# Kernel tuning notes

Measured on AMD Instinct MI355X. Metric: run time of the kernel, lower is better.

The kernel has to match this reference:

```python
import jax, jax.numpy as jnp
import numpy as np

DIM = 128; D_STATE = 16; D_CONV = 4; EXPAND = 2
D_INNER = DIM * EXPAND            # 256
DT_RANK = (DIM + 15) // 16        # 8
B, H, W = 2, 56, 56


def _ln(x, w, b):
    m = jnp.mean(x, -1, keepdims=True)
    v = jnp.var(x, -1, keepdims=True)
    return (x - m) * jax.lax.rsqrt(v + 1e-5) * w + b


def _mamba(x, in_w, conv_w, conv_b, xproj_w, dt_w, dt_b, A_log, Dp, out_w):
    # x: (B, L, DIM)
    Bb, L, _ = x.shape
    xz = x @ in_w.T                                   # (B,L,2*D_INNER)
    xi, z = jnp.split(xz, 2, axis=-1)
    # causal depthwise conv1d (pad left d_conv-1, truncate to L)
    xc = jnp.transpose(xi, (0, 2, 1))                 # (B,D_INNER,L)
    xc = jax.lax.conv_general_dilated(
        xc, conv_w, (1,), [(D_CONV - 1, 0)],
        dimension_numbers=('NCH', 'OIH', 'NCH'),
        feature_group_count=D_INNER) + conv_b[None, :, None]
    xs = jax.nn.silu(jnp.transpose(xc, (0, 2, 1)))    # (B,L,D_INNER)
    dbl = xs @ xproj_w.T                              # (B,L,DT_RANK+2*D_STATE)
    dt = jax.nn.softplus(dbl[..., :DT_RANK] @ dt_w.T + dt_b)   # (B,L,D_INNER)
    Bc = dbl[..., DT_RANK:DT_RANK + D_STATE]          # (B,L,D_STATE)
    Cc = dbl[..., DT_RANK + D_STATE:]                 # (B,L,D_STATE)
    A = -jnp.exp(A_log)                               # (D_INNER,D_STATE)
    dA = jnp.exp(dt[..., None] * A)                   # (B,L,D_INNER,D_STATE)
    dBu = (dt * xs)[..., None] * Bc[:, :, None, :]    # (B,L,D_INNER,D_STATE)

    def step(h, inp):
        a, bu, c = inp
        h = a * h + bu                                # (B,D_INNER,D_STATE)
        return h, jnp.einsum('bdn,bn->bd', h, c)

    h0 = jnp.zeros((Bb, D_INNER, D_STATE), x.dtype)
    _, ys = jax.lax.scan(step, h0, (jnp.moveaxis(dA, 1, 0),
                                    jnp.moveaxis(dBu, 1, 0),
                                    jnp.moveaxis(Cc, 1, 0)))
    y = jnp.moveaxis(ys, 0, 1) + xs * Dp              # (B,L,D_INNER)
    y = y * jax.nn.silu(z)
    return y @ out_w.T                                # (B,L,DIM)


def _forward(x, norm_h_w, norm_h_b, norm_v_w, norm_v_b,
             dw_w, dw_b, pw_w, pw_b,
             h_in_w, h_conv_w, h_conv_b, h_xproj_w, h_dt_w, h_dt_b, h_A_log, h_D, h_out_w,
             v_in_w, v_conv_w, v_conv_b, v_xproj_w, v_dt_w, v_dt_b, v_A_log, v_D, v_out_w,
             ca_fc1_w, ca_fc2_w):
    Bb, C, Hh, Ww = x.shape
    # local branch: depthwise 3x3 + GELU + 1x1
    lf = jax.lax.conv_general_dilated(
        x, dw_w, (1, 1), [(1, 1), (1, 1)],
        dimension_numbers=('NCHW', 'OIHW', 'NCHW'),
        feature_group_count=C) + dw_b[None, :, None, None]
    lf = jax.nn.gelu(lf, approximate=False)
    lf = jnp.einsum('bchw,oc->bohw', lf, pw_w[:, :, 0, 0]) + pw_b[None, :, None, None]
    # horizontal scan: row-major tokens
    xh = _ln(x.reshape(Bb, C, Hh * Ww).transpose(0, 2, 1), norm_h_w, norm_h_b)
    oh = _mamba(xh, h_in_w, h_conv_w, h_conv_b, h_xproj_w, h_dt_w, h_dt_b,
                h_A_log, h_D, h_out_w)
    oh = oh.transpose(0, 2, 1).reshape(Bb, C, Hh, Ww)
    # vertical scan: column-major tokens
    xv = _ln(jnp.transpose(x, (0, 1, 3, 2)).reshape(Bb, C, Ww * Hh).transpose(0, 2, 1),
             norm_v_w, norm_v_b)
    ov = _mamba(xv, v_in_w, v_conv_w, v_conv_b, v_xproj_w, v_dt_w, v_dt_b,
                v_A_log, v_D, v_out_w)
    ov = jnp.transpose(ov.transpose(0, 2, 1).reshape(Bb, C, Ww, Hh), (0, 1, 3, 2))
    fused = oh + ov + lf
    # channel attention
    y = jnp.mean(fused, axis=(2, 3))                  # (B,C)
    y = jax.nn.sigmoid(jax.nn.relu(y @ ca_fc1_w.T) @ ca_fc2_w.T)
    return fused * y[:, :, None, None] + x


def setup_inputs() -> dict:
    key = jax.random.key(0)
    ks = iter(jax.random.split(key, 64))
    def nrm(shape, scale):
        return jax.random.normal(next(ks), shape, jnp.float32) * scale
    d = {}
    d['x'] = nrm((B, DIM, H, W), 1.0)
    d['norm_h_w'] = jnp.ones((DIM,), jnp.float32); d['norm_h_b'] = jnp.zeros((DIM,), jnp.float32)
    d['norm_v_w'] = jnp.ones((DIM,), jnp.float32); d['norm_v_b'] = jnp.zeros((DIM,), jnp.float32)
    d['dw_w'] = nrm((DIM, 1, 3, 3), 1.0 / 3.0)
    d['dw_b'] = jnp.zeros((DIM,), jnp.float32)
    d['pw_w'] = nrm((DIM, DIM, 1, 1), DIM ** -0.5)
    d['pw_b'] = jnp.zeros((DIM,), jnp.float32)
    for p in ('h', 'v'):
        d[p + '_in_w'] = nrm((2 * D_INNER, DIM), DIM ** -0.5)
        d[p + '_conv_w'] = nrm((D_INNER, 1, D_CONV), D_CONV ** -0.5)
        d[p + '_conv_b'] = jnp.zeros((D_INNER,), jnp.float32)
        d[p + '_xproj_w'] = nrm((DT_RANK + 2 * D_STATE, D_INNER), D_INNER ** -0.5)
        d[p + '_dt_w'] = nrm((D_INNER, DT_RANK), DT_RANK ** -0.5)
        d[p + '_dt_b'] = jnp.full((D_INNER,), -2.0, jnp.float32)  # small positive dt
        d[p + '_A_log'] = jnp.log(jnp.tile(jnp.arange(1, D_STATE + 1, dtype=jnp.float32), (D_INNER, 1)))
        d[p + '_D'] = jnp.ones((D_INNER,), jnp.float32)
        d[p + '_out_w'] = nrm((DIM, D_INNER), D_INNER ** -0.5)
    d['ca_fc1_w'] = nrm((DIM // 4, DIM), DIM ** -0.5)
    d['ca_fc2_w'] = nrm((DIM, DIM // 4), (DIM // 4) ** -0.5)
    return d


def reference(x, norm_h_w, norm_h_b, norm_v_w, norm_v_b,
              dw_w, dw_b, pw_w, pw_b,
              h_in_w, h_conv_w, h_conv_b, h_xproj_w, h_dt_w, h_dt_b, h_A_log, h_D, h_out_w,
              v_in_w, v_conv_w, v_conv_b, v_xproj_w, v_dt_w, v_dt_b, v_A_log, v_D, v_out_w,
              ca_fc1_w, ca_fc2_w):
    return _forward(x, norm_h_w, norm_h_b, norm_v_w, norm_v_b,
                    dw_w, dw_b, pw_w, pw_b,
                    h_in_w, h_conv_w, h_conv_b, h_xproj_w, h_dt_w, h_dt_b, h_A_log, h_D, h_out_w,
                    v_in_w, v_conv_w, v_conv_b, v_xproj_w, v_dt_w, v_dt_b, v_A_log, v_D, v_out_w,
                    ca_fc1_w, ca_fc2_w)
```

## Files before the change

kernel.cpp:

```cpp
#include <hip/hip_runtime.h>
#include <hip/hip_bf16.h>

typedef __hip_bfloat16 bf16;
__device__ __forceinline__ float b2f(bf16 v){ return __bfloat162float(v); }
__device__ __forceinline__ bf16 f2b(float v){ return __float2bfloat16(v); }

typedef __attribute__((ext_vector_type(8))) short frag_ab;
typedef __attribute__((ext_vector_type(4))) float frag_cd;
typedef __attribute__((ext_vector_type(4))) short short4v;

__device__ __forceinline__ frag_ab ld_frag_2xb64(const bf16* p){
  union { frag_ab f; short4v h[2]; } u;
  u.h[0] = *reinterpret_cast<const short4v*>(p);
  u.h[1] = *reinterpret_cast<const short4v*>(p+4);
  return u.f;
}

#define LLEN 3136
#define BATCH 2
#define NCHUNK 49
#define LC 64

__global__ void k_dwconv_gelu(const float* __restrict__ x, const float* __restrict__ dww,
                              const float* __restrict__ dwb, bf16* __restrict__ tmp,
                              float* __restrict__ YMEAN){
  int bc = blockIdx.x;
  int c = bc & 127;
  if (bc == 0 && blockIdx.y == 0 && threadIdx.x < 256) YMEAN[threadIdx.x] = 0.f;
  const float* xp = x + (size_t)bc*LLEN;
  float w[9];
  #pragma unroll
  for (int i=0;i<9;i++) w[i] = dww[c*9+i];
  float bias = dwb[c];
  int pstart = blockIdx.y * 784;
  int pend = pstart + 784;
  for (int p = pstart + threadIdx.x; p < pend; p += 256){
    int i = p/56, j = p%56;
    float acc = bias;
    #pragma unroll
    for (int a=0;a<3;a++){
      int ii = i + a - 1;
      if (ii < 0 || ii >= 56) continue;
      #pragma unroll
      for (int bb=0;bb<3;bb++){
        int jj = j + bb - 1;
        if (jj < 0 || jj >= 56) continue;
        acc += w[a*3+bb] * xp[ii*56+jj];
      }
    }
    float g = 0.5f*acc*(1.0f + erff(acc*0.70710678118654752f));
    tmp[(size_t)bc*LLEN + p] = f2b(g);
  }
}

__global__ void k_ln(const float* __restrict__ x, const float* nhw_, const float* nhb_,
                     const float* nvw_, const float* nvb_, bf16* __restrict__ xln){
  __shared__ float sx[128][57];
  __shared__ float smean[56], srstd[56];
  __shared__ float wh[128], bh[128], wv_[128], bv_[128];
  int h = blockIdx.x; int b = blockIdx.y;
  int tid = threadIdx.x;
  if (tid < 128){ wh[tid]=nhw_[tid]; bh[tid]=nhb_[tid];
                  wv_[tid]=nvw_[tid]; bv_[tid]=nvb_[tid]; }
  for (int idx = tid; idx < 128*56; idx += 256){
    int c = idx / 56, w = idx % 56;
    sx[c][w] = x[((size_t)(b*128+c))*LLEN + h*56 + w];
  }
  __syncthreads();
  if (tid < 56){
    float s=0.f, s2=0.f;
    for (int c=0;c<128;c++){ float v = sx[c][tid]; s+=v; s2+=v*v; }
    float m = s*(1.f/128.f);
    float var = s2*(1.f/128.f) - m*m;
    smean[tid]=m; srstd[tid]=rsqrtf(var+1e-5f);
  }
  __syncthreads();
  bf16* outh = xln;
  bf16* outv = xln + (size_t)BATCH*LLEN*128;
  for (int idx = tid; idx < 56*128; idx += 256){
    int w = idx >> 7, c = idx & 127;
    float v = (sx[c][w]-smean[w])*srstd[w];
    outh[((size_t)b*LLEN + h*56 + w)*128 + c] = f2b(v*wh[c]+bh[c]);
    outv[((size_t)b*LLEN + w*56 + h)*128 + c] = f2b(v*wv_[c]+bv_[c]);
  }
}

__global__ void k_inproj(const bf16* __restrict__ xln, const float* __restrict__ hw,
                         const float* __restrict__ vw, bf16* __restrict__ XI, bf16* __restrict__ Z){
  int dir = blockIdx.z;
  const bf16* A = xln + (size_t)dir*BATCH*LLEN*128;
  const float* W = dir ? vw : hw;
  int m0 = blockIdx.x*64, n0 = blockIdx.y*64;
  __shared__ __align__(16) bf16 sA[64][136];
  __shared__ __align__(16) bf16 sW[64][136];
  int tid = threadIdx.x;
  #pragma unroll
  for (int r=0;r<4;r++){
    int idx = tid + r*256;
    int row = idx >> 4, c8 = (idx & 15)*8;
    *reinterpret_cast<float4*>(&sA[row][c8]) =
        *reinterpret_cast<const float4*>(&A[(size_t)(m0+row)*128 + c8]);
  }
  #pragma unroll
  for (int r=0;r<8;r++){
    int idx = tid + r*256;
    int row = idx >> 5, c4 = (idx & 31)*4;
    float4 w4 = *reinterpret_cast<const float4*>(&W[(size_t)(n0+row)*128 + c4]);
    bf16 t4[4] = {f2b(w4.x), f2b(w4.y), f2b(w4.z), f2b(w4.w)};
    *reinterpret_cast<double*>(&sW[row][c4]) = *reinterpret_cast<double*>(t4);
  }
  __syncthreads();
  int wv2 = tid >> 6, lane = tid & 63;
  int qd = lane >> 4, mr = lane & 15;
  frag_cd acc[4] = {};
  #pragma unroll
  for (int k0=0;k0<128;k0+=32){
    frag_ab af = *reinterpret_cast<frag_ab*>(&sA[wv2*16+mr][k0+qd*8]);
    #pragma unroll
    for (int t=0;t<4;t++){
      frag_ab bfr = *reinterpret_cast<frag_ab*>(&sW[t*16+mr][k0+qd*8]);
      acc[t] = __builtin_amdgcn_mfma_f32_16x16x32_bf16(af, bfr, acc[t], 0, 0, 0);
    }
  }
  bf16* dst = (n0 < 256) ? XI : Z;
  int nb = n0 & 255;
  size_t dslab = (size_t)dir*BATCH*LLEN*256;
  #pragma unroll
  for (int t=0;t<4;t++)
    #pragma unroll
    for (int r=0;r<4;r++){
      int row = m0 + wv2*16 + qd*4 + r;
      int col = nb + t*16 + mr;
      dst[dslab + (size_t)row*256 + col] = f2b(acc[t][r]);
    }
}

__global__ void k_conv(const bf16* __restrict__ XI, const float* hw, const float* hb,
                       const float* vw, const float* vb, bf16* __restrict__ XS2){
  int dir = blockIdx.z;
  int b = blockIdx.y;
  int bd = dir*BATCH + b;
  int l0 = blockIdx.x * 32;
  const bf16* XId = XI + (size_t)bd*LLEN*256;
  const float* cw = dir ? vw : hw;
  const float* cb = dir ? vb : hb;
  __shared__ float sxi[35][256];
  int tid = threadIdx.x;
  for (int r = 0; r < 35; r++){
    int l = l0 - 3 + r;
    sxi[r][tid] = (l >= 0) ? b2f(XId[(size_t)l*256 + tid]) : 0.f;
  }
  __syncthreads();
  float w0=cw[tid*4], w1=cw[tid*4+1], w2=cw[tid*4+2], w3=cw[tid*4+3];
  float bias = cb[tid];
  size_t x2base = ((size_t)bd*16 + (tid>>4))*LLEN;
  int c16 = tid & 15;
  for (int ll=0; ll<32; ll++){
    float acc = bias + w0*sxi[ll][tid] + w1*sxi[ll+1][tid] + w2*sxi[ll+2][tid] + w3*sxi[ll+3][tid];
    float s = acc / (1.f + __expf(-acc));
    XS2[(x2base + l0 + ll)*16 + c16] = f2b(s);
  }
}

__global__ void k_dbl(const bf16* __restrict__ XS2, const float* __restrict__ hx,
                      const float* __restrict__ vx,
                      const float* hdw, const float* vdw, const float* hdb, const float* vdb,
                      const float* hA, const float* vA,
                      bf16* __restrict__ DT2, float* __restrict__ Bf, float* __restrict__ Cf,
                      float* __restrict__ Pbuf, float* __restrict__ Hbuf){
  int m0 = blockIdx.x*64;
  int bd = m0 / LLEN;
  int l0m = m0 % LLEN;
  int ck = l0m / LC;
  int dirq = bd >> 1;
  const float* W = dirq ? vx : hx;
  __shared__ __align__(16) bf16 sA[64][264];
  __shared__ __align__(16) bf16 sW[48][264];
  __shared__ float sdbl[64][49];
  int tid = threadIdx.x;
  #pragma unroll
  for (int r=0;r<8;r++){
    int idx = tid + r*256;
    int row = idx >> 5, c8 = (idx & 31)*8;
    size_t src = (((size_t)bd*16 + (c8>>4))*LLEN + l0m + row)*16 + (c8&15);
    *reinterpret_cast<float4*>(&sA[row][c8]) =
        *reinterpret_cast<const float4*>(&XS2[src]);
  }
  #pragma unroll
  for (int r=0;r<12;r++){
    int idx = tid + r*256;
    int row = idx >> 6, c4 = (idx & 63)*4;
    bf16 t4[4] = {f2b(0.f), f2b(0.f), f2b(0.f), f2b(0.f)};
    if (row < 40){
      float4 w4 = *reinterpret_cast<const float4*>(&W[(size_t)row*256 + c4]);
      t4[0]=f2b(w4.x); t4[1]=f2b(w4.y); t4[2]=f2b(w4.z); t4[3]=f2b(w4.w);
    }
    *reinterpret_cast<double*>(&sW[row][c4]) = *reinterpret_cast<double*>(t4);
  }
  __syncthreads();
  int wv2 = tid >> 6, lane = tid & 63;
  int qd = lane >> 4, mr = lane & 15;
  frag_cd acc[3] = {};
  #pragma unroll
  for (int k0=0;k0<256;k0+=32){
    frag_ab af = *reinterpret_cast<frag_ab*>(&sA[wv2*16+mr][k0+qd*8]);
    #pragma unroll
    for (int t=0;t<3;t++){
      frag_ab bfr = *reinterpret_cast<frag_ab*>(&sW[t*16+mr][k0+qd*8]);
      acc[t] = __builtin_amdgcn_mfma_f32_16x16x32_bf16(af, bfr, acc[t], 0, 0, 0);
    }
  }
  #pragma unroll
  for (int t=0;t<3;t++)
    #pragma unroll
    for (int r=0;r<4;r++){
      int col = t*16 + mr;
      if (col < 40) sdbl[wv2*16 + qd*4 + r][col] = acc[t][r];
    }
  __syncthreads();
  const float* dtw = dirq ? vdw : hdw;
  const float* dtb = dirq ? vdb : hdb;
  const float* Alog = dirq ? vA : hA;
  float w8[8];
  #pragma unroll
  for (int r=0;r<8;r++) w8[r] = dtw[tid*8+r];
  float biasv = dtb[tid];
  float Aq[16];
  #pragma unroll
  for (int n=0;n<16;n++) Aq[n] = -__expf(Alog[tid*16+n]);
  float hst[16] = {};
  float Pst[16];
  #pragma unroll
  for (int n=0;n<16;n++) Pst[n] = 1.f;
  size_t d2base = ((size_t)bd*16 + (tid>>4))*LLEN + l0m;
  int c16 = tid & 15;
  for (int row=0; row<64; row++){
    float a = biasv;
    #pragma unroll
    for (int r=0;r<8;r++) a += sdbl[row][r]*w8[r];
    float sv = (a > 20.f) ? a : __logf(1.f + __expf(a));
    bf16 svb16 = f2b(sv);
    DT2[(d2base + row)*16 + c16] = svb16;
    float svb = b2f(svb16);
    float u = b2f(sA[row][tid]);
    float au = svb*u;
    #pragma unroll
    for (int n=0;n<16;n++){
      float dA = __expf(svb * Aq[n]);
      hst[n] = dA*hst[n] + au*sdbl[row][8+n];
      Pst[n] *= dA;
    }
  }
  size_t pbase = (((size_t)bd*16 + (tid>>4))*NCHUNK + ck)*256 + (size_t)(tid&15)*16;
  #pragma unroll
  for (int n=0;n<16;n++){ Pbuf[pbase+n] = Pst[n]; Hbuf[pbase+n] = hst[n]; }
  #pragma unroll
  for (int r=0;r<8;r++){
    int idx = tid + r*256;
    int row = idx >> 5, o = idx & 31;
    float v = sdbl[row][8+o];
    size_t rr = (size_t)(m0+row)*16;
    if (o < 16) Bf[rr + o] = v;
    else        Cf[rr + (o-16)] = v;
  }
}

__global__ void k_scan2(const float* __restrict__ Pbuf, float* __restrict__ Hbuf){
  int q = blockIdx.x;
  int tid = threadIdx.x;
  float carry = 0.f;
  for (int k=0;k<NCHUNK;k++){
    size_t idx = ((size_t)q*NCHUNK + k)*256 + tid;
    float Pv = Pbuf[idx];
    float He = Hbuf[idx];
    Hbuf[idx] = carry;
    carry = Pv*carry + He;
  }
}

__global__ void k_scan3(const bf16* __restrict__ DT2, const bf16* __restrict__ XS2,
                        const float* __restrict__ Bc, const float* __restrict__ Cc,
                        const float* hA, const float* vA,
                        const float* __restrict__ Hbuf, bf16* __restrict__ ys){
  int bd = blockIdx.z;
  int g  = blockIdx.y;
  int ck = blockIdx.x;
  int l0 = ck*LC;
  const float* Bd = Bc + (size_t)bd*LLEN*16;
  const float* Cd = Cc + (size_t)bd*LLEN*16;
  bf16* yd = ys + (size_t)bd*LLEN*256;
  const float* Alog = (bd >> 1) ? vA : hA;
  int tid = threadIdx.x;
  int dl = tid >> 4, n = tid & 15;
  float A = -__expf(Alog[(g*16+dl)*16+n]);
  __shared__ float sdt[LC][16], sxs[LC][16], sB[LC][16], sC[LC][16];
  __shared__ __align__(16) float sp2[16][276];
  size_t base2 = (((size_t)bd*16 + g)*LLEN + l0)*16;
  #pragma unroll
  for (int r=0;r<4;r++){
    int idx = tid + r*256;
    sdt[idx>>4][idx&15] = b2f(DT2[base2 + idx]);
    sxs[idx>>4][idx&15] = b2f(XS2[base2 + idx]);
    (&sB[0][0])[idx] = Bd[(size_t)l0*16 + idx];
    (&sC[0][0])[idx] = Cd[(size_t)l0*16 + idx];
  }
  size_t sidx = (((size_t)bd*16 + g)*NCHUNK + ck)*256 + tid;
  float h = Hbuf[sidx];
  __syncthreads();
  int i_local = tid >> 4;
  int c16 = tid & 15;
  for (int i0=0; i0<LC; i0+=16){
    #pragma unroll
    for (int ii=0;ii<16;ii++){
      int i = i0 + ii;
      float a = sdt[i][dl];
      float u = sxs[i][dl];
      float dA = __expf(a * A);
      h = dA*h + (a*u)*sB[i][n];
      sp2[ii][tid] = h * sC[i][n];
    }
    __syncthreads();
    const float* row = &sp2[i_local][c16*16];
    float s = 0.f;
    #pragma unroll
    for (int k=0;k<4;k++){
      float4 v = *reinterpret_cast<const float4*>(row + k*4);
      s += v.x + v.y + v.z + v.w;
    }
    yd[(size_t)(l0+i0+i_local)*256 + g*16 + c16] = f2b(s);
    __syncthreads();
  }
}

__global__ void k_outgemm(const bf16* __restrict__ ys, const bf16* __restrict__ XS2,
                          const bf16* __restrict__ Z, const float* __restrict__ hD,
                          const float* __restrict__ vD, const float* __restrict__ how,
                          const float* __restrict__ vow, bf16* __restrict__ OD){
  int dir = blockIdx.z;
  size_t slab = (size_t)dir*BATCH*LLEN*256;
  const float* W = dir ? vow : how;
  const float* Dw = dir ? vD : hD;
  bf16* od = OD + (size_t)dir*BATCH*LLEN*128;
  int m0 = blockIdx.x*64, n0 = blockIdx.y*64;
  int bd = dir*2 + m0/LLEN;
  int lbase = m0 % LLEN;
  __shared__ __align__(16) bf16 sA[64][136];
  __shared__ __align__(16) bf16 sW[64][136];
  int tid = threadIdx.x;
  int wv2 = tid >> 6, lane = tid & 63;
  int qd = lane >> 4, mr = lane & 15;
  frag_cd acc[4] = {};
  for (int kc=0; kc<256; kc+=128){
    __syncthreads();
    #pragma unroll
    for (int r=0;r<4;r++){
      int idx = tid + r*256;
      int row = idx >> 4, c8 = (idx & 15)*8;
      int k = kc + c8;
      size_t e = slab + (size_t)(m0+row)*256 + k;
      size_t e2 = (((size_t)bd*16 + (k>>4))*LLEN + lbase + row)*16 + (k&15);
      bf16 yb[8], xb[8], zb[8], ob[8];
      *reinterpret_cast<float4*>(yb) = *reinterpret_cast<const float4*>(&ys[e]);
      *reinterpret_cast<float4*>(xb) = *reinterpret_cast<const float4*>(&XS2[e2]);
      *reinterpret_cast<float4*>(zb) = *reinterpret_cast<const float4*>(&Z[e]);
      #pragma unroll
      for (int j=0;j<8;j++){
        float Dv = Dw[k + j];
        float yv = b2f(yb[j]) + b2f(xb[j])*Dv;
        float zv = b2f(zb[j]);
        ob[j] = f2b(yv * (zv/(1.f+__expf(-zv))));
      }
      *reinterpret_cast<float4*>(&sA[row][c8]) = *reinterpret_cast<float4*>(ob);
    }
    #pragma unroll
    for (int r=0;r<8;r++){
      int idx = tid + r*256;
      int row = idx >> 5, c4 = (idx & 31)*4;
      float4 w4 = *reinterpret_cast<const float4*>(&W[(size_t)(n0+row)*256 + kc + c4]);
      bf16 t4[4] = {f2b(w4.x), f2b(w4.y), f2b(w4.z), f2b(w4.w)};
      *reinterpret_cast<double*>(&sW[row][c4]) = *reinterpret_cast<double*>(t4);
    }
    __syncthreads();
    #pragma unroll
    for (int k0=0;k0<128;k0+=32){
      frag_ab af = *reinterpret_cast<frag_ab*>(&sA[wv2*16+mr][k0+qd*8]);
      #pragma unroll
      for (int t=0;t<4;t++){
        frag_ab bfr = *reinterpret_cast<frag_ab*>(&sW[t*16+mr][k0+qd*8]);
        acc[t] = __builtin_amdgcn_mfma_f32_16x16x32_bf16(af, bfr, acc[t], 0, 0, 0);
      }
    }
  }
  #pragma unroll
  for (int t=0;t<4;t++)
    #pragma unroll
    for (int r=0;r<4;r++){
      int row = m0 + wv2*16 + qd*4 + r;
      int col = n0 + t*16 + mr;
      od[(size_t)row*128 + col] = f2b(acc[t][r]);
    }
}

__global__ void k_pwcomb(const bf16* __restrict__ tmp, const float* __restrict__ pww,
                         const float* __restrict__ pwb, const bf16* __restrict__ OD,
                         float* __restrict__ fused, float* __restrict__ YMEAN){
  int p0 = blockIdx.x * 64;
  int m0 = blockIdx.y * 64;
  int b  = blockIdx.z;
  const bf16* T = tmp + (size_t)b*128*LLEN;
  const bf16* od0 = OD + (size_t)b*LLEN*128;
  const bf16* od1 = OD + (size_t)(BATCH + b)*LLEN*128;
  __shared__ __align__(16) bf16 sA[64][136];
  __shared__ __align__(16) bf16 sBt[64][132];
  __shared__ float sOD[64][65];
  int tid = threadIdx.x;
  #pragma unroll
  for (int r=0;r<8;r++){
    int idx = tid + r*256;
    int row = idx >> 5, c4 = (idx & 31)*4;
    float4 w4 = *reinterpret_cast<const float4*>(&pww[(size_t)(m0+row)*128 + c4]);
    bf16 t4[4] = {f2b(w4.x), f2b(w4.y), f2b(w4.z), f2b(w4.w)};
    *reinterpret_cast<double*>(&sA[row][c4]) = *reinterpret_cast<double*>(t4);
  }
  #pragma unroll
  for (int r=0;r<8;r++){
    int idx = tid + r*256;
    int c = idx >> 4, p4 = (idx & 15)*4;
    union { double d; bf16 v[4]; } u;
    u.d = *reinterpret_cast<const double*>(&T[(size_t)c*LLEN + p0 + p4]);
    #pragma unroll
    for (int j=0;j<4;j++) sBt[p4+j][c] = u.v[j];
  }
  #pragma unroll
  for (int r=0;r<8;r++){
    int idx = tid + r*256;
    int prow = idx >> 5, mp = (idx & 31)*2;
    int p = p0 + prow;
    int pi = p/56, pj = p%56;
    int pt = pj*56 + pi;
    bf16 a0[2], a1[2];
    *reinterpret_cast<float*>(a0) = *reinterpret_cast<const float*>(&od0[(size_t)p*128 + m0 + mp]);
    *reinterpret_cast<float*>(a1) = *reinterpret_cast<const float*>(&od1[(size_t)pt*128 + m0 + mp]);
    sOD[prow][mp]   = b2f(a0[0]) + b2f(a1[0]);
    sOD[prow][mp+1] = b2f(a0[1]) + b2f(a1[1]);
  }
  __syncthreads();
  int wv2 = tid >> 6, lane = tid & 63;
  int qd = lane >> 4, mr = lane & 15;
  frag_cd acc[4] = {};
  #pragma unroll
  for (int k0=0;k0<128;k0+=32){
    frag_ab af = *reinterpret_cast<frag_ab*>(&sA[wv2*16+mr][k0+qd*8]);
    #pragma unroll
    for (int t=0;t<4;t++){
      frag_ab bfr = ld_frag_2xb64(&sBt[t*16+mr][k0+qd*8]);
      acc[t] = __builtin_amdgcn_mfma_f32_16x16x32_bf16(af, bfr, acc[t], 0, 0, 0);
    }
  }
  #pragma unroll
  for (int r=0;r<4;r++){
    int m = m0 + wv2*16 + qd*4 + r;
    float bias = pwb[m];
    float s = 0.f;
    #pragma unroll
    for (int t=0;t<4;t++){
      int p = p0 + t*16 + mr;
      float val = acc[t][r] + bias + sOD[t*16+mr][m - m0];
      fused[((size_t)b*128 + m)*LLEN + p] = val;
      s += val;
    }
    s += __shfl_xor(s, 1, 16);
    s += __shfl_xor(s, 2, 16);
    s += __shfl_xor(s, 4, 16);
    s += __shfl_xor(s, 8, 16);
    if (mr == 0) atomicAdd(&YMEAN[b*128 + m], s);
  }
}

__global__ void k_final_gate(const float* __restrict__ fused, const float* __restrict__ YMEAN,
                             const float* __restrict__ fc1, const float* __restrict__ fc2,
                             const float* __restrict__ x, float* __restrict__ out){
  int bc = blockIdx.y;
  int b = bc >> 7, c = bc & 127;
  __shared__ float ym[128], s1[32];
  __shared__ float gsh;
  int tid = threadIdx.x;
  if (tid < 128) ym[tid] = YMEAN[b*128 + tid] * (1.f/(float)LLEN);
  __syncthreads();
  if (tid < 32){
    float a = 0.f;
    for (int cc=0;cc<128;cc++) a += ym[cc]*fc1[tid*128+cc];
    s1[tid] = fmaxf(a, 0.f);
  }
  __syncthreads();
  if (tid == 0){
    float a = 0.f;
    #pragma unroll
    for (int j=0;j<32;j++) a += s1[j]*fc2[c*32+j];
    gsh = 1.f/(1.f+__expf(-a));
  }
  __syncthreads();
  float g = gsh;
  int p = blockIdx.x*256 + tid;
  if (p < LLEN){
    size_t i = (size_t)bc*LLEN + p;
    out[i] = fused[i]*g + x[i];
  }
}

extern "C" void kernel_launch(void* const* d_in, const int* in_sizes, int n_in,
                              void* d_out, int out_size, void* d_ws, size_t ws_size,
                              hipStream_t stream) {
  const float* x      = (const float*)d_in[0];
  const float* nhw    = (const float*)d_in[1];
  const float* nhb    = (const float*)d_in[2];
  const float* nvw    = (const float*)d_in[3];
  const float* nvb    = (const float*)d_in[4];
  const float* dww    = (const float*)d_in[5];
  const float* dwb    = (const float*)d_in[6];
  const float* pww    = (const float*)d_in[7];
  const float* pwb    = (const float*)d_in[8];
  const float* h_inw  = (const float*)d_in[9];
  const float* h_cw   = (const float*)d_in[10];
  const float* h_cb   = (const float*)d_in[11];
  const float* h_xw   = (const float*)d_in[12];
  const float* h_dtw  = (const float*)d_in[13];
  const float* h_dtb  = (const float*)d_in[14];
  const float* h_Al   = (const float*)d_in[15];
  const float* h_D    = (const float*)d_in[16];
  const float* h_ow   = (const float*)d_in[17];
  const float* v_inw  = (const float*)d_in[18];
  const float* v_cw   = (const float*)d_in[19];
  const float* v_cb   = (const float*)d_in[20];
  const float* v_xw   = (const float*)d_in[21];
  const float* v_dtw  = (const float*)d_in[22];
  const float* v_dtb  = (const float*)d_in[23];
  const float* v_Al   = (const float*)d_in[24];
  const float* v_D    = (const float*)d_in[25];
  const float* v_ow   = (const float*)d_in[26];
  const float* fc1    = (const float*)d_in[27];
  const float* fc2    = (const float*)d_in[28];

  float* FUSED = (float*)d_out;
  float* out   = (float*)d_out;

  char* base = (char*)d_ws;
  bf16*  XLN   = (bf16*)(base + 1605632);
  bf16*  DT2   = (bf16*)(base + 0);
  bf16*  OD    = (bf16*)(base + 0);
  bf16*  XI    = (bf16*)(base + 6422528);
  bf16*  YS    = (bf16*)(base + 6422528);
  float* Pbuf  = (float*)(base + 6422528);
  bf16*  Z     = (bf16*)(base + 12845056);
  bf16*  XS2   = (bf16*)(base + 19267584);
  float* Bf    = (float*)(base + 25690112);
  float* Cf    = (float*)(base + 26492928);
  float* Hbuf  = (float*)(base + 27295744);
  float* YMEAN = (float*)(base + 30507008);
  bf16*  TMP   = (bf16*)(base + 30508032);

  k_dwconv_gelu<<<dim3(BATCH*128,4), dim3(256), 0, stream>>>(x, dww, dwb, TMP, YMEAN);
  k_ln<<<dim3(56,BATCH), dim3(256), 0, stream>>>(x, nhw, nhb, nvw, nvb, XLN);
  k_inproj<<<dim3(98,8,2), dim3(256), 0, stream>>>(XLN, h_inw, v_inw, XI, Z);
  k_conv<<<dim3(98,BATCH,2), dim3(256), 0, stream>>>(XI, h_cw, h_cb, v_cw, v_cb, XS2);
  k_dbl<<<dim3(196), dim3(256), 0, stream>>>(XS2, h_xw, v_xw, h_dtw, v_dtw, h_dtb, v_dtb,
                                             h_Al, v_Al, DT2, Bf, Cf, Pbuf, Hbuf);
  k_scan2<<<dim3(64), dim3(256), 0, stream>>>(Pbuf, Hbuf);
  k_scan3<<<dim3(NCHUNK,16,4), dim3(256), 0, stream>>>(DT2, XS2, Bf, Cf, h_Al, v_Al, Hbuf, YS);
  k_outgemm<<<dim3(98,2,2), dim3(256), 0, stream>>>(YS, XS2, Z, h_D, v_D, h_ow, v_ow, OD);
  k_pwcomb<<<dim3(49,2,BATCH), dim3(256), 0, stream>>>(TMP, pww, pwb, OD, FUSED, YMEAN);
  k_final_gate<<<dim3(13,256), dim3(256), 0, stream>>>(FUSED, YMEAN, fc1, fc2, x, out);
}
```

Baseline: 257.8 us.

## Reuse A tiles across N tiles in in-proj and out-proj GEMMs

```diff
diff --git a/kernel.cpp b/kernel.cpp
--- a/kernel.cpp
+++ b/kernel.cpp
@@ -90,7 +90,8 @@
   int dir = blockIdx.z;
   const bf16* A = xln + (size_t)dir*BATCH*LLEN*128;
   const float* W = dir ? vw : hw;
-  int m0 = blockIdx.x*64, n0 = blockIdx.y*64;
+  int m0 = blockIdx.x*64;
+  int npair = blockIdx.y*128;
   __shared__ __align__(16) bf16 sA[64][136];
   __shared__ __align__(16) bf16 sW[64][136];
   int tid = threadIdx.x;
@@ -101,38 +102,44 @@
     *reinterpret_cast<float4*>(&sA[row][c8]) =
         *reinterpret_cast<const float4*>(&A[(size_t)(m0+row)*128 + c8]);
   }
-  #pragma unroll
-  for (int r=0;r<8;r++){
-    int idx = tid + r*256;
-    int row = idx >> 5, c4 = (idx & 31)*4;
-    float4 w4 = *reinterpret_cast<const float4*>(&W[(size_t)(n0+row)*128 + c4]);
-    bf16 t4[4] = {f2b(w4.x), f2b(w4.y), f2b(w4.z), f2b(w4.w)};
-    *reinterpret_cast<double*>(&sW[row][c4]) = *reinterpret_cast<double*>(t4);
-  }
-  __syncthreads();
   int wv2 = tid >> 6, lane = tid & 63;
   int qd = lane >> 4, mr = lane & 15;
-  frag_cd acc[4] = {};
-  #pragma unroll
-  for (int k0=0;k0<128;k0+=32){
-    frag_ab af = *reinterpret_cast<frag_ab*>(&sA[wv2*16+mr][k0+qd*8]);
-    #pragma unroll
-    for (int t=0;t<4;t++){
-      frag_ab bfr = *reinterpret_cast<frag_ab*>(&sW[t*16+mr][k0+qd*8]);
-      acc[t] = __builtin_amdgcn_mfma_f32_16x16x32_bf16(af, bfr, acc[t], 0, 0, 0);
-    }
-  }
-  bf16* dst = (n0 < 256) ? XI : Z;
-  int nb = n0 & 255;
+  bf16* dst = (npair < 256) ? XI : Z;
+  int nbase0 = npair & 255;
   size_t dslab = (size_t)dir*BATCH*LLEN*256;
   #pragma unroll
-  for (int t=0;t<4;t++)
-    #pragma unroll
-    for (int r=0;r<4;r++){
-      int row = m0 + wv2*16 + qd*4 + r;
-      int col = nb + t*16 + mr;
-      dst[dslab + (size_t)row*256 + col] = f2b(acc[t][r]);
-    }
+  for (int nt=0; nt<2; nt++){
+    int n0 = npair + nt*64;
+    __syncthreads();
+    #pragma unroll
+    for (int r=0;r<8;r++){
+      int idx = tid + r*256;
+      int row = idx >> 5, c4 = (idx & 31)*4;
+      float4 w4 = *reinterpret_cast<const float4*>(&W[(size_t)(n0+row)*128 + c4]);
+      bf16 t4[4] = {f2b(w4.x), f2b(w4.y), f2b(w4.z), f2b(w4.w)};
+      *reinterpret_cast<double*>(&sW[row][c4]) = *reinterpret_cast<double*>(t4);
+    }
+    __syncthreads();
+    frag_cd acc[4] = {};
+    #pragma unroll
+    for (int k0=0;k0<128;k0+=32){
+      frag_ab af = *reinterpret_cast<frag_ab*>(&sA[wv2*16+mr][k0+qd*8]);
+      #pragma unroll
+      for (int t=0;t<4;t++){
+        frag_ab bfr = *reinterpret_cast<frag_ab*>(&sW[t*16+mr][k0+qd*8]);
+        acc[t] = __builtin_amdgcn_mfma_f32_16x16x32_bf16(af, bfr, acc[t], 0, 0, 0);
+      }
+    }
+    int nb = nbase0 + nt*64;
+    #pragma unroll
+    for (int t=0;t<4;t++)
+      #pragma unroll
+      for (int r=0;r<4;r++){
+        int row = m0 + wv2*16 + qd*4 + r;
+        int col = nb + t*16 + mr;
+        dst[dslab + (size_t)row*256 + col] = f2b(acc[t][r]);
+      }
+  }
 }
 
 __global__ void k_conv(const bf16* __restrict__ XI, const float* hw, const float* hb,
@@ -336,69 +343,71 @@
                           const bf16* __restrict__ Z, const float* __restrict__ hD,
                           const float* __restrict__ vD, const float* __restrict__ how,
                           const float* __restrict__ vow, bf16* __restrict__ OD){
-  int dir = blockIdx.z;
+  int dir = blockIdx.y;
   size_t slab = (size_t)dir*BATCH*LLEN*256;
   const float* W = dir ? vow : how;
   const float* Dw = dir ? vD : hD;
   bf16* od = OD + (size_t)dir*BATCH*LLEN*128;
-  int m0 = blockIdx.x*64, n0 = blockIdx.y*64;
+  int m0 = blockIdx.x*32;
   int bd = dir*2 + m0/LLEN;
   int lbase = m0 % LLEN;
-  __shared__ __align__(16) bf16 sA[64][136];
-  __shared__ __align__(16) bf16 sW[64][136];
-  int tid = threadIdx.x;
+  __shared__ __align__(16) bf16 sA[32][264];
+  __shared__ __align__(16) bf16 sW[64][264];
+  int tid = threadIdx.x;
+  #pragma unroll
+  for (int r=0;r<4;r++){
+    int idx = tid + r*256;
+    int row = idx >> 5, c8 = (idx & 31)*8;
+    size_t e = slab + (size_t)(m0+row)*256 + c8;
+    size_t e2 = (((size_t)bd*16 + (c8>>4))*LLEN + lbase + row)*16 + (c8&15);
+    bf16 yb[8], xb[8], zb[8], ob[8];
+    *reinterpret_cast<float4*>(yb) = *reinterpret_cast<const float4*>(&ys[e]);
+    *reinterpret_cast<float4*>(xb) = *reinterpret_cast<const float4*>(&XS2[e2]);
+    *reinterpret_cast<float4*>(zb) = *reinterpret_cast<const float4*>(&Z[e]);
+    #pragma unroll
+    for (int j=0;j<8;j++){
+      float Dv = Dw[c8 + j];
+      float yv = b2f(yb[j]) + b2f(xb[j])*Dv;
+      float zv = b2f(zb[j]);
+      ob[j] = f2b(yv * (zv/(1.f+__expf(-zv))));
+    }
+    *reinterpret_cast<float4*>(&sA[row][c8]) = *reinterpret_cast<float4*>(ob);
+  }
   int wv2 = tid >> 6, lane = tid & 63;
   int qd = lane >> 4, mr = lane & 15;
-  frag_cd acc[4] = {};
-  for (int kc=0; kc<256; kc+=128){
+  int msub = wv2 & 1, tpair = (wv2 >> 1)*2;
+  #pragma unroll
+  for (int nh=0; nh<2; nh++){
+    int n0 = nh*64;
     __syncthreads();
     #pragma unroll
-    for (int r=0;r<4;r++){
+    for (int r=0;r<16;r++){
       int idx = tid + r*256;
-      int row = idx >> 4, c8 = (idx & 15)*8;
-      int k = kc + c8;
-      size_t e = slab + (size_t)(m0+row)*256 + k;
-      size_t e2 = (((size_t)bd*16 + (k>>4))*LLEN + lbase + row)*16 + (k&15);
-      bf16 yb[8], xb[8], zb[8], ob[8];
-      *reinterpret_cast<float4*>(yb) = *reinterpret_cast<const float4*>(&ys[e]);
-      *reinterpret_cast<float4*>(xb) = *reinterpret_cast<const float4*>(&XS2[e2]);
-      *reinterpret_cast<float4*>(zb) = *reinterpret_cast<const float4*>(&Z[e]);
-      #pragma unroll
-      for (int j=0;j<8;j++){
-        float Dv = Dw[k + j];
-        float yv = b2f(yb[j]) + b2f(xb[j])*Dv;
-        float zv = b2f(zb[j]);
-        ob[j] = f2b(yv * (zv/(1.f+__expf(-zv))));
-      }
-      *reinterpret_cast<float4*>(&sA[row][c8]) = *reinterpret_cast<float4*>(ob);
-    }
-    #pragma unroll
-    for (int r=0;r<8;r++){
-      int idx = tid + r*256;
-      int row = idx >> 5, c4 = (idx & 31)*4;
-      float4 w4 = *reinterpret_cast<const float4*>(&W[(size_t)(n0+row)*256 + kc + c4]);
+      int row = idx >> 6, c4 = (idx & 63)*4;
+      float4 w4 = *reinterpret_cast<const float4*>(&W[(size_t)(n0+row)*256 + c4]);
       bf16 t4[4] = {f2b(w4.x), f2b(w4.y), f2b(w4.z), f2b(w4.w)};
       *reinterpret_cast<double*>(&sW[row][c4]) = *reinterpret_cast<double*>(t4);
     }
     __syncthreads();
-    #pragma unroll
-    for (int k0=0;k0<128;k0+=32){
-      frag_ab af = *reinterpret_cast<frag_ab*>(&sA[wv2*16+mr][k0+qd*8]);
+    frag_cd acc[2] = {};
+    #pragma unroll
+    for (int k0=0;k0<256;k0+=32){
+      frag_ab af = *reinterpret_cast<frag_ab*>(&sA[msub*16+mr][k0+qd*8]);
       #pragma unroll
-      for (int t=0;t<4;t++){
-        frag_ab bfr = *reinterpret_cast<frag_ab*>(&sW[t*16+mr][k0+qd*8]);
-        acc[t] = __builtin_amdgcn_mfma_f32_16x16x32_bf16(af, bfr, acc[t], 0, 0, 0);
+      for (int i=0;i<2;i++){
+        frag_ab bfr = *reinterpret_cast<frag_ab*>(&sW[(tpair+i)*16+mr][k0+qd*8]);
+        acc[i] = __builtin_amdgcn_mfma_f32_16x16x32_bf16(af, bfr, acc[i], 0, 0, 0);
       }
     }
-  }
-  #pragma unroll
-  for (int t=0;t<4;t++)
-    #pragma unroll
-    for (int r=0;r<4;r++){
-      int row = m0 + wv2*16 + qd*4 + r;
-      int col = n0 + t*16 + mr;
-      od[(size_t)row*128 + col] = f2b(acc[t][r]);
-    }
+    #pragma unroll
+    for (int i=0;i<2;i++)
+      #pragma unroll
+      for (int r=0;r<4;r++){
+        int row = m0 + msub*16 + qd*4 + r;
+        int col = n0 + (tpair+i)*16 + mr;
+        od[(size_t)row*128 + col] = f2b(acc[i][r]);
+      }
+  }
 }
 
 __global__ void k_pwcomb(const bf16* __restrict__ tmp, const float* __restrict__ pww,
@@ -561,13 +570,13 @@
 
   k_dwconv_gelu<<<dim3(BATCH*128,4), dim3(256), 0, stream>>>(x, dww, dwb, TMP, YMEAN);
   k_ln<<<dim3(56,BATCH), dim3(256), 0, stream>>>(x, nhw, nhb, nvw, nvb, XLN);
-  k_inproj<<<dim3(98,8,2), dim3(256), 0, stream>>>(XLN, h_inw, v_inw, XI, Z);
+  k_inproj<<<dim3(98,4,2), dim3(256), 0, stream>>>(XLN, h_inw, v_inw, XI, Z);
   k_conv<<<dim3(98,BATCH,2), dim3(256), 0, stream>>>(XI, h_cw, h_cb, v_cw, v_cb, XS2);
   k_dbl<<<dim3(196), dim3(256), 0, stream>>>(XS2, h_xw, v_xw, h_dtw, v_dtw, h_dtb, v_dtb,
                                              h_Al, v_Al, DT2, Bf, Cf, Pbuf, Hbuf);
   k_scan2<<<dim3(64), dim3(256), 0, stream>>>(Pbuf, Hbuf);
   k_scan3<<<dim3(NCHUNK,16,4), dim3(256), 0, stream>>>(DT2, XS2, Bf, Cf, h_Al, v_Al, Hbuf, YS);
-  k_outgemm<<<dim3(98,2,2), dim3(256), 0, stream>>>(YS, XS2, Z, h_D, v_D, h_ow, v_ow, OD);
+  k_outgemm<<<dim3(196,2), dim3(256), 0, stream>>>(YS, XS2, Z, h_D, v_D, h_ow, v_ow, OD);
   k_pwcomb<<<dim3(49,2,BATCH), dim3(256), 0, stream>>>(TMP, pww, pwb, OD, FUSED, YMEAN);
   k_final_gate<<<dim3(13,256), dim3(256), 0, stream>>>(FUSED, YMEAN, fc1, fc2, x, out);
 }
```

New measurement: 252.7 us. -2.0%, faster.
